# Performance work log

Measured on AMD Instinct MI355X. Metric: run time of the kernel, lower is better.

Reference implementation:

```python
import jax, jax.numpy as jnp
import numpy as np

N = 50000   # nodes
E = 600000  # edges (avg degree ~12)
R = 8       # num_relations = 2 * n_speakers**2, n_speakers=2
B = 32      # num_bases = args.batch_size
GD, H1, H2 = 128, 128, 128


def setup_inputs() -> dict:
    key = jax.random.key(0)
    ks = jax.random.split(key, 16)
    w = lambda k, shape: jax.random.normal(k, shape, jnp.float32) * 0.05
    return {
        "node_features": jax.random.normal(ks[0], (N, GD), jnp.float32),
        "edge_index": jax.random.randint(ks[1], (2, E), 0, N),
        "edge_norm": jax.random.uniform(ks[2], (E,), jnp.float32),
        "edge_type": jax.random.randint(ks[3], (E,), 0, R),
        "basis": w(ks[4], (B, GD, H1)),
        "comp": w(ks[5], (R, B)),
        "root": w(ks[6], (GD, H1)),
        "bias1": jnp.zeros((H1,), jnp.float32),
        "w_key": w(ks[7], (H1, H2)),
        "b_key": jnp.zeros((H2,), jnp.float32),
        "w_query": w(ks[8], (H1, H2)),
        "b_query": jnp.zeros((H2,), jnp.float32),
        "w_value": w(ks[9], (H1, H2)),
        "b_value": jnp.zeros((H2,), jnp.float32),
        "w_skip": w(ks[10], (H1, H2)),
        "b_skip": jnp.zeros((H2,), jnp.float32),
    }


def reference(node_features, edge_index, edge_norm, edge_type, basis, comp,
              root, bias1, w_key, b_key, w_query, b_query, w_value, b_value,
              w_skip, b_skip):
    n = node_features.shape[0]
    r = comp.shape[0]
    src, dst = edge_index[0], edge_index[1]

    # ---- RGCNConv (basis decomposition, per-relation mean aggregation) ----
    W = jnp.einsum('rb,bio->rio', comp, basis)            # [R, GD, H1]
    xW = jnp.einsum('ni,rio->rno', node_features, W)      # [R, N, H1]
    msg = xW[edge_type, src]                              # [E, H1]
    seg = edge_type * n + dst                             # combined (relation, dst) segment id
    agg = jax.ops.segment_sum(msg, seg, num_segments=r * n).reshape(r, n, -1)
    cnt = jax.ops.segment_sum(jnp.ones(msg.shape[0], jnp.float32), seg,
                              num_segments=r * n).reshape(r, n, 1)
    h = (agg / jnp.maximum(cnt, 1.0)).sum(0) + node_features @ root + bias1

    # ---- ResGatedGraphConv: sigmoid(k_i + q_j) * v_j, sum-aggregated + skip ----
    k = h @ w_key + b_key
    q = h @ w_query + b_query
    v = h @ w_value + b_value
    m = jax.nn.sigmoid(k[dst] + q[src]) * v[src]          # [E, H2]
    out = jax.ops.segment_sum(m, dst, num_segments=n) + h @ w_skip + b_skip
    return out
```

## Files before the change

### kernel.cpp

```cpp
#include <hip/hip_runtime.h>
#include <stdint.h>

#define GD 128
#define H1 128
#define H2 128
#define NBASES 32
#define NREL 8
#define KA 1152

typedef __attribute__((ext_vector_type(8))) short bf16x8;
typedef __attribute__((ext_vector_type(4))) float f32x4;

static inline size_t align256(size_t x){ return (x + 255) & ~(size_t)255; }

__device__ __forceinline__ float bf2f(uint32_t u16){
  union { uint32_t u; float f; } c; c.u = (u16 & 0xffffu) << 16; return c.f;
}
__device__ __forceinline__ unsigned short f2bf(float f){
  union { float f; uint32_t u; } c; c.f = f;
  uint32_t u = c.u;
  u += 0x7fffu + ((u >> 16) & 1u);
  return (unsigned short)(u >> 16);
}
__device__ __forceinline__ uint32_t pkbf(float a, float b){
  union { float f; uint32_t u; } ca, cb; ca.f = a; cb.f = b;
  return __builtin_amdgcn_perm(cb.u + 0x8000u, ca.u + 0x8000u, 0x07060302u);
}

__device__ __forceinline__ void async_copy16(void* lds_dst, const void* gsrc){
  __builtin_amdgcn_global_load_lds(
      (const __attribute__((address_space(1))) uint32_t*)gsrc,
      (__attribute__((address_space(3))) uint32_t*)lds_dst, 16, 0, 0);
}

__global__ void k_prep(const float* __restrict__ comp, const float* __restrict__ basis,
                       const float* __restrict__ root, unsigned short* __restrict__ Bht,
                       const float* __restrict__ wk, const float* __restrict__ wq,
                       const float* __restrict__ wv, const float* __restrict__ wsk,
                       const float* __restrict__ bk, const float* __restrict__ bq,
                       const float* __restrict__ bv, const float* __restrict__ bs,
                       unsigned short* __restrict__ B2t, float* __restrict__ Bb,
                       const float4* __restrict__ x, uint2* __restrict__ xout, int cnt4,
                       uint32_t* __restrict__ xpadz, int npadz,
                       const int* __restrict__ edst, const int* __restrict__ etyp,
                       int* __restrict__ cnt, int E, int n){
  const float LOG2E = 1.4426950408889634f;
  int b = blockIdx.x, t = threadIdx.x;
  if (b < 576){
    int idx = b*256 + t;
    int row = idx >> 7, i = idx & 127;
    int r = row >> 7, o = row & 127;
    float v;
    if (r < 8){
      float acc = 0.f;
      #pragma unroll
      for (int bb = 0; bb < NBASES; ++bb)
        acc += comp[r*NBASES + bb] * basis[((size_t)bb*GD + i)*H1 + o];
      v = acc;
    } else {
      v = root[(size_t)i*H1 + o];
    }
    Bht[(size_t)o*KA + r*128 + i] = f2bf(v);
  } else if (b < 576 + 256){
    int idx = (b - 576)*256 + t;
    int c = idx / H1, k = idx % H1;
    const float* w = (c < 128) ? wk : (c < 256) ? wq : (c < 384) ? wv : wsk;
    float val = w[(size_t)k*H2 + (c & 127)];
    if (c < 256) val *= LOG2E;
    B2t[idx] = f2bf(val);
    if (idx < 512){
      const float* bia = (idx < 128) ? bk : (idx < 256) ? bq : (idx < 384) ? bv : bs;
      float bval = bia[idx & 127];
      if (idx < 256) bval *= LOG2E;
      Bb[idx] = bval;
    }
  } else {
    int cb = b - (576 + 256);
    int ncastb = (cnt4 + 255) >> 8;
    if (cb < ncastb){
      int i = cb*256 + t;
      if (i < cnt4){
        float4 v = x[i];
        uint2 o; o.x = pkbf(v.x, v.y); o.y = pkbf(v.z, v.w);
        xout[i] = o;
      }
    } else if (cb < ncastb + 12){
      int i = (cb - ncastb)*256 + t;
      if (i < npadz) xpadz[i] = 0u;
    } else {
      int e = (cb - ncastb - 12)*256 + t;
      if (e < E) atomicAdd(&cnt[etyp[e]*n + edst[e]], 1);
    }
  }
}

__global__ void k_scanA(const int* __restrict__ deg, int* __restrict__ off,
                        int* __restrict__ btot, int len){
  __shared__ int wsum[16];
  int t = threadIdx.x, lane = t & 63, w = t >> 6;
  int i0 = blockIdx.x*8192 + t*8;
  int v[8];
  if (i0 + 7 < len){
    int4 va = *(const int4*)(deg + i0);
    int4 vb = *(const int4*)(deg + i0 + 4);
    v[0]=va.x; v[1]=va.y; v[2]=va.z; v[3]=va.w;
    v[4]=vb.x; v[5]=vb.y; v[6]=vb.z; v[7]=vb.w;
  } else {
    #pragma unroll
    for (int u = 0; u < 8; ++u) v[u] = (i0+u < len) ? deg[i0+u] : 0;
  }
  int s[8]; s[0] = v[0];
  #pragma unroll
  for (int u = 1; u < 8; ++u) s[u] = s[u-1] + v[u];
  int x = s[7];
  #pragma unroll
  for (int d = 1; d < 64; d <<= 1){
    int u = __shfl_up(x, d, 64);
    if (lane >= d) x += u;
  }
  if (lane == 63) wsum[w] = x;
  __syncthreads();
  if (t < 16){
    int y = wsum[t];
    #pragma unroll
    for (int d = 1; d < 16; d <<= 1){
      int u = __shfl_up(y, d, 16);
      if (t >= d) y += u;
    }
    wsum[t] = y;
  }
  __syncthreads();
  int woff = (w > 0) ? wsum[w-1] : 0;
  int excl = woff + x - s[7];
  #pragma unroll
  for (int u = 0; u < 8; ++u)
    if (i0+u < len) off[i0+u] = excl + s[u] - v[u];
  if (t == 0) btot[blockIdx.x] = wsum[15];
}

__global__ void k_scanB(const int* __restrict__ btot, int* __restrict__ off,
                        int* __restrict__ cursor, int len, int sentinel){
  int t = threadIdx.x, bid = blockIdx.x;
  int add = 0;
  for (int j = 0; j < bid; ++j) add += btot[j];
  int i0 = bid*8192 + t*8;
  #pragma unroll
  for (int u = 0; u < 8; ++u){
    int i = i0 + u;
    if (i < len){ int val = off[i] + add; off[i] = val; cursor[i] = val; }
  }
  if (bid == 0 && t == 0) off[len] = sentinel;
}

__global__ void k_scatter_rd(const int* __restrict__ src, const int* __restrict__ dst,
                             const int* __restrict__ typ, int* __restrict__ cursor,
                             int* __restrict__ pk, int E, int n){
  int e = blockIdx.x*blockDim.x + threadIdx.x;
  if (e >= E) return;
  int pos = atomicAdd(&cursor[typ[e]*n + dst[e]], 1);
  pk[pos] = src[e];
}

__global__ void k_agg(const int* __restrict__ off_rd, const int* __restrict__ pk_rd,
                      const uint32_t* __restrict__ x32, unsigned short* __restrict__ A2,
                      int n, int npad){
  int wid = blockIdx.x*(blockDim.x >> 6) + (threadIdx.x >> 6);
  int lane = threadIdx.x & 63;
  if (wid >= npad) return;
  uint32_t* arow = (uint32_t*)(A2 + (size_t)wid*1024);
  if (wid >= n){
    #pragma unroll
    for (int u = 0; u < 8; ++u) arow[u*64 + lane] = 0u;
    return;
  }
  int r8 = lane & 7;
  int o_r = off_rd[(size_t)r8*n + wid];
  int e_r = off_rd[(size_t)r8*n + wid + 1];
  int c_r = e_r - o_r;
  float ic_r = (c_r > 0) ? __builtin_amdgcn_rcpf((float)c_r) : 0.f;
  int c0_ = __builtin_amdgcn_readlane(c_r, 0), c1_ = __builtin_amdgcn_readlane(c_r, 1);
  int c2_ = __builtin_amdgcn_readlane(c_r, 2), c3_ = __builtin_amdgcn_readlane(c_r, 3);
  int c4_ = __builtin_amdgcn_readlane(c_r, 4), c5_ = __builtin_amdgcn_readlane(c_r, 5);
  int c6_ = __builtin_amdgcn_readlane(c_r, 6), c7_ = __builtin_amdgcn_readlane(c_r, 7);
  int o0_ = __builtin_amdgcn_readlane(o_r, 0), o1_ = __builtin_amdgcn_readlane(o_r, 1);
  int o2_ = __builtin_amdgcn_readlane(o_r, 2), o3_ = __builtin_amdgcn_readlane(o_r, 3);
  int o4_ = __builtin_amdgcn_readlane(o_r, 4), o5_ = __builtin_amdgcn_readlane(o_r, 5);
  int o6_ = __builtin_amdgcn_readlane(o_r, 6), o7_ = __builtin_amdgcn_readlane(o_r, 7);
  int p1 = c0_, p2 = p1 + c1_, p3 = p2 + c2_, p4 = p3 + c3_;
  int p5 = p4 + c4_, p6 = p5 + c5_, p7 = p6 + c6_, dg = p7 + c7_;

  int cr = 0;
  float a0 = 0.f, a1 = 0.f;

#define FLUSH(RK)                                                               \
  {                                                                             \
    float ic = __int_as_float(__builtin_amdgcn_readlane(__float_as_int(ic_r), cr)); \
    arow[cr*64 + lane] = pkbf(a0*ic, a1*ic);                                    \
    for (int q = cr + 1; q < (RK); ++q) arow[q*64 + lane] = 0u;                 \
    cr = (RK); a0 = 0.f; a1 = 0.f;                                              \
  }

  for (int jb = 0; jb < dg; jb += 64){
    int i = jb + lane;
    int adj = o0_, rel = 0;
    adj = (i >= p1) ? (o1_ - p1) : adj;  rel += (i >= p1);
    adj = (i >= p2) ? (o2_ - p2) : adj;  rel += (i >= p2);
    adj = (i >= p3) ? (o3_ - p3) : adj;  rel += (i >= p3);
    adj = (i >= p4) ? (o4_ - p4) : adj;  rel += (i >= p4);
    adj = (i >= p5) ? (o5_ - p5) : adj;  rel += (i >= p5);
    adj = (i >= p6) ? (o6_ - p6) : adj;  rel += (i >= p6);
    adj = (i >= p7) ? (o7_ - p7) : adj;  rel += (i >= p7);
    int m = dg - jb; if (m > 64) m = 64;
    int pj = (lane < m) ? pk_rd[adj + i] : 0;
    int jj = 0;
    for (; jj + 8 <= m; jj += 8){
      uint32_t g[8];
      #pragma unroll
      for (int k = 0; k < 8; ++k){
        int sN = __builtin_amdgcn_readlane(pj, jj + k);
        g[k] = x32[(size_t)(uint32_t)sN*64 + lane];
      }
      #pragma unroll
      for (int k = 0; k < 8; ++k){
        int rk = __builtin_amdgcn_readlane(rel, jj + k);
        if (rk != cr) FLUSH(rk);
        a0 += bf2f(g[k]); a1 += bf2f(g[k] >> 16);
      }
    }
    for (; jj < m; jj += 4){
      int lim = m - 1;
      uint32_t g[4];
      #pragma unroll
      for (int k = 0; k < 4; ++k){
        int tt = jj + k; if (tt > lim) tt = lim;
        int sN = __builtin_amdgcn_readlane(pj, tt);
        g[k] = x32[(size_t)(uint32_t)sN*64 + lane];
      }
      #pragma unroll
      for (int k = 0; k < 4; ++k){
        int tt = jj + k;
        if (tt < m){
          int rk = __builtin_amdgcn_readlane(rel, tt);
          if (rk != cr) FLUSH(rk);
          a0 += bf2f(g[k]); a1 += bf2f(g[k] >> 16);
        }
      }
    }
  }
  FLUSH(8)
#undef FLUSH
}

__launch_bounds__(256)
__global__ void k_hgemm(const unsigned short* __restrict__ A, const unsigned short* __restrict__ xb,
                        const unsigned short* __restrict__ Bt,
                        const float* __restrict__ bias1, unsigned short* __restrict__ h){
  __shared__ char lds[16896];
  int t = threadIdx.x, lane = t & 63, wave = t >> 6;
  int row0 = blockIdx.x * 128;
  int mrow = lane & 15, quad = lane >> 4;
  int wrow = (wave & 1) * 64, wcol = (wave >> 1) * 64;
  int s = (mrow >> 1) & 3;
  int colsw = (((t & 3) ^ ((t >> 3) & 3)) << 3);

  const unsigned short* Asrc = A  + (size_t)(row0 + (t >> 2))*1024 + colsw;
  const unsigned short* Xsrc = xb + (size_t)(row0 + (t >> 2))*GD   + colsw;
  const unsigned short* Bsrc = Bt + (size_t)(t >> 2)*KA + colsw;
  char* ldsw = lds + wave*1024;

  int aoff = (wrow + mrow)*64 + ((quad ^ s) << 4);
  int boff = 8192 + (wcol + mrow)*64 + ((quad ^ s) << 4);

  f32x4 acc[4][4];
  #pragma unroll
  for (int i = 0; i < 4; ++i)
    #pragma unroll
    for (int j = 0; j < 4; ++j) acc[i][j] = (f32x4){0.f,0.f,0.f,0.f};

  for (int kt = 0; kt < KA; kt += 32){
    const unsigned short* a0p = (kt < 1024) ? (Asrc + kt)
                                            : (Xsrc + (kt - 1024));
    const unsigned short* a1p = (kt < 1024) ? (Asrc + (size_t)64*1024 + kt)
                                            : (Xsrc + (size_t)64*GD + (kt - 1024));
    __syncthreads();
    async_copy16(ldsw,         a0p);
    async_copy16(ldsw + 4096,  a1p);
    async_copy16(ldsw + 8192,  Bsrc + kt);
    async_copy16(ldsw + 12288, Bsrc + (size_t)64*KA + kt);
    __syncthreads();
    bf16x8 af[4], bf[4];
    #pragma unroll
    for (int i = 0; i < 4; ++i) af[i] = *(const bf16x8*)(lds + aoff + i*1024);
    #pragma unroll
    for (int j = 0; j < 4; ++j) bf[j] = *(const bf16x8*)(lds + boff + j*1024);
    #pragma unroll
    for (int i = 0; i < 4; ++i)
      #pragma unroll
      for (int j = 0; j < 4; ++j)
        acc[i][j] = __builtin_amdgcn_mfma_f32_16x16x32_bf16(af[i], bf[j], acc[i][j], 0, 0, 0);
  }
  float bc[4];
  #pragma unroll
  for (int j = 0; j < 4; ++j) bc[j] = bias1[wcol + j*16 + mrow];
  #pragma unroll
  for (int p = 0; p < 2; ++p){
    __syncthreads();
    if ((wave & 1) == p){
      #pragma unroll
      for (int j = 0; j < 4; ++j){
        int col = wcol + j*16 + mrow;
        #pragma unroll
        for (int i = 0; i < 4; ++i)
          #pragma unroll
          for (int rg = 0; rg < 4; ++rg){
            int rl = i*16 + quad*4 + rg;
            *(unsigned short*)(lds + rl*264 + col*2) = f2bf(acc[i][j][rg] + bc[j]);
          }
      }
    }
    __syncthreads();
    uint32_t vv[16];
    #pragma unroll
    for (int u = 0; u < 8; ++u)
      *(uint2*)&vv[u*2] = *(const uint2*)(lds + lane*264 + wave*64 + u*8);
    unsigned short* gp = h + (size_t)(row0 + p*64 + lane)*H1 + wave*32;
    #pragma unroll
    for (int u = 0; u < 4; ++u)
      *(uint4*)(gp + u*8) = *(const uint4*)&vv[u*4];
  }
}

__launch_bounds__(256)
__global__ void k_gemm2(const unsigned short* __restrict__ A, const unsigned short* __restrict__ Bt,
                        const float* __restrict__ Bb, unsigned short* __restrict__ kqv,
                        unsigned short* __restrict__ skipb){
  __shared__ char lds[16896];
  int t = threadIdx.x, lane = t & 63, wave = t >> 6;
  int row0 = blockIdx.x * 128;
  int c0 = blockIdx.y * 128;
  int mrow = lane & 15, quad = lane >> 4;
  int wrow = (wave & 1) * 64, wcol = (wave >> 1) * 64;
  int s = (mrow >> 1) & 3;

  const unsigned short* Asrc = A + (size_t)(row0 + (t >> 2))*H1 + (((t & 3) ^ ((t >> 3) & 3)) << 3);
  const unsigned short* Bsrc = Bt + (size_t)(c0 + (t >> 2))*H1 + (((t & 3) ^ ((t >> 3) & 3)) << 3);
  char* ldsw = lds + wave*1024;

  int aoff = (wrow + mrow)*64 + ((quad ^ s) << 4);
  int boff = 8192 + (wcol + mrow)*64 + ((quad ^ s) << 4);

  f32x4 acc[4][4];
  #pragma unroll
  for (int i = 0; i < 4; ++i)
    #pragma unroll
    for (int j = 0; j < 4; ++j) acc[i][j] = (f32x4){0.f,0.f,0.f,0.f};

  #pragma unroll
  for (int kt = 0; kt < H1; kt += 32){
    __syncthreads();
    async_copy16(ldsw,         Asrc + kt);
    async_copy16(ldsw + 4096,  Asrc + (size_t)64*H1 + kt);
    async_copy16(ldsw + 8192,  Bsrc + kt);
    async_copy16(ldsw + 12288, Bsrc + (size_t)64*H1 + kt);
    __syncthreads();
    bf16x8 af[4], bf[4];
    #pragma unroll
    for (int i = 0; i < 4; ++i) af[i] = *(const bf16x8*)(lds + aoff + i*1024);
    #pragma unroll
    for (int j = 0; j < 4; ++j) bf[j] = *(const bf16x8*)(lds + boff + j*1024);
    #pragma unroll
    for (int i = 0; i < 4; ++i)
      #pragma unroll
      for (int j = 0; j < 4; ++j)
        acc[i][j] = __builtin_amdgcn_mfma_f32_16x16x32_bf16(af[i], bf[j], acc[i][j], 0, 0, 0);
  }
  float bc[4];
  #pragma unroll
  for (int j = 0; j < 4; ++j) bc[j] = Bb[c0 + wcol + j*16 + mrow];
  unsigned short* dstb; size_t ldu;
  if (c0 < 384){ dstb = kqv + c0; ldu = 384; } else { dstb = skipb; ldu = 128; }
  #pragma unroll
  for (int p = 0; p < 2; ++p){
    __syncthreads();
    if ((wave & 1) == p){
      #pragma unroll
      for (int j = 0; j < 4; ++j){
        int col = wcol + j*16 + mrow;
        #pragma unroll
        for (int i = 0; i < 4; ++i)
          #pragma unroll
          for (int rg = 0; rg < 4; ++rg){
            int rl = i*16 + quad*4 + rg;
            *(unsigned short*)(lds + rl*264 + col*2) = f2bf(acc[i][j][rg] + bc[j]);
          }
      }
    }
    __syncthreads();
    uint32_t vv[16];
    #pragma unroll
    for (int u = 0; u < 8; ++u)
      *(uint2*)&vv[u*2] = *(const uint2*)(lds + lane*264 + wave*64 + u*8);
    unsigned short* gp = dstb + (size_t)(row0 + p*64 + lane)*ldu + wave*32;
    #pragma unroll
    for (int u = 0; u < 4; ++u)
      *(uint4*)(gp + u*8) = *(const uint4*)&vv[u*4];
  }
}

__global__ void k_edge2(const int* __restrict__ off_rd, const int* __restrict__ pk_rd,
                        const unsigned short* __restrict__ kqv,
                        const unsigned short* __restrict__ skipb,
                        float* __restrict__ out, int n){
  int wid = blockIdx.x*(blockDim.x >> 6) + (threadIdx.x >> 6);
  int lane = threadIdx.x & 63;
  if (wid >= n) return;
  const uint32_t* kv32 = (const uint32_t*)kqv;
  int r = lane & 7;
  int o_r = off_rd[(size_t)r*n + wid];
  int e_r = off_rd[(size_t)r*n + wid + 1];
  int c_r = e_r - o_r;
  int c0_ = __builtin_amdgcn_readlane(c_r, 0), c1_ = __builtin_amdgcn_readlane(c_r, 1);
  int c2_ = __builtin_amdgcn_readlane(c_r, 2), c3_ = __builtin_amdgcn_readlane(c_r, 3);
  int c4_ = __builtin_amdgcn_readlane(c_r, 4), c5_ = __builtin_amdgcn_readlane(c_r, 5);
  int c6_ = __builtin_amdgcn_readlane(c_r, 6), c7_ = __builtin_amdgcn_readlane(c_r, 7);
  int o0_ = __builtin_amdgcn_readlane(o_r, 0), o1_ = __builtin_amdgcn_readlane(o_r, 1);
  int o2_ = __builtin_amdgcn_readlane(o_r, 2), o3_ = __builtin_amdgcn_readlane(o_r, 3);
  int o4_ = __builtin_amdgcn_readlane(o_r, 4), o5_ = __builtin_amdgcn_readlane(o_r, 5);
  int o6_ = __builtin_amdgcn_readlane(o_r, 6), o7_ = __builtin_amdgcn_readlane(o_r, 7);
  int p1 = c0_, p2 = p1 + c1_, p3 = p2 + c2_, p4 = p3 + c3_;
  int p5 = p4 + c4_, p6 = p5 + c5_, p7 = p6 + c6_, dg = p7 + c7_;

  uint32_t ku = kv32[(size_t)wid*192 + lane];
  float k0 = bf2f(ku), k1 = bf2f(ku >> 16);
  float a0 = 0.f, a1 = 0.f;
  for (int jb = 0; jb < dg; jb += 64){
    int i = jb + lane;
    int adj = o0_;
    adj = (i >= p1) ? (o1_ - p1) : adj;
    adj = (i >= p2) ? (o2_ - p2) : adj;
    adj = (i >= p3) ? (o3_ - p3) : adj;
    adj = (i >= p4) ? (o4_ - p4) : adj;
    adj = (i >= p5) ? (o5_ - p5) : adj;
    adj = (i >= p6) ? (o6_ - p6) : adj;
    adj = (i >= p7) ? (o7_ - p7) : adj;
    int m = dg - jb; if (m > 64) m = 64;
    int pj = (lane < m) ? pk_rd[adj + i] : 0;
    int jj = 0;
    for (; jj + 8 <= m; jj += 8){
      uint32_t qg[8], vg[8];
      #pragma unroll
      for (int k = 0; k < 8; ++k){
        int s = __builtin_amdgcn_readlane(pj, jj + k);
        const uint32_t* rowp = kv32 + (size_t)s*192 + lane;
        qg[k] = rowp[64];
        vg[k] = rowp[128];
      }
      #pragma unroll
      for (int k = 0; k < 8; ++k){
        float qq0 = bf2f(qg[k]), qq1 = bf2f(qg[k] >> 16);
        float vv0 = bf2f(vg[k]), vv1 = bf2f(vg[k] >> 16);
        float g0 = __builtin_amdgcn_rcpf(1.f + __builtin_amdgcn_exp2f(-(k0 + qq0)));
        float g1 = __builtin_amdgcn_rcpf(1.f + __builtin_amdgcn_exp2f(-(k1 + qq1)));
        a0 += g0*vv0; a1 += g1*vv1;
      }
    }
    for (; jj + 4 <= m; jj += 4){
      uint32_t qg[4], vg[4];
      #pragma unroll
      for (int k = 0; k < 4; ++k){
        int s = __builtin_amdgcn_readlane(pj, jj + k);
        const uint32_t* rowp = kv32 + (size_t)s*192 + lane;
        qg[k] = rowp[64];
        vg[k] = rowp[128];
      }
      #pragma unroll
      for (int k = 0; k < 4; ++k){
        float qq0 = bf2f(qg[k]), qq1 = bf2f(qg[k] >> 16);
        float vv0 = bf2f(vg[k]), vv1 = bf2f(vg[k] >> 16);
        float g0 = __builtin_amdgcn_rcpf(1.f + __builtin_amdgcn_exp2f(-(k0 + qq0)));
        float g1 = __builtin_amdgcn_rcpf(1.f + __builtin_amdgcn_exp2f(-(k1 + qq1)));
        a0 += g0*vv0; a1 += g1*vv1;
      }
    }
    for (; jj < m; ++jj){
      int s = __builtin_amdgcn_readlane(pj, jj);
      const uint32_t* rowp = kv32 + (size_t)s*192 + lane;
      uint32_t qg = rowp[64], vg = rowp[128];
      float qq0 = bf2f(qg), qq1 = bf2f(qg >> 16);
      float vv0 = bf2f(vg), vv1 = bf2f(vg >> 16);
      float g0 = __builtin_amdgcn_rcpf(1.f + __builtin_amdgcn_exp2f(-(k0 + qq0)));
      float g1 = __builtin_amdgcn_rcpf(1.f + __builtin_amdgcn_exp2f(-(k1 + qq1)));
      a0 += g0*vv0; a1 += g1*vv1;
    }
  }
  uint32_t sk = ((const uint32_t*)skipb)[(size_t)wid*64 + lane];
  float2 cur; cur.x = a0 + bf2f(sk); cur.y = a1 + bf2f(sk >> 16);
  ((float2*)(out + (size_t)wid*H2))[lane] = cur;
}

extern "C" void kernel_launch(void* const* d_in, const int* in_sizes, int n_in,
                              void* d_out, int out_size, void* d_ws, size_t ws_size,
                              hipStream_t stream){
  const float* x     = (const float*)d_in[0];
  const int*   eidx  = (const int*)  d_in[1];
  const int*   etype = (const int*)  d_in[3];
  const float* basis = (const float*)d_in[4];
  const float* comp  = (const float*)d_in[5];
  const float* root  = (const float*)d_in[6];
  const float* bias1 = (const float*)d_in[7];
  const float* wk    = (const float*)d_in[8];
  const float* bk    = (const float*)d_in[9];
  const float* wq    = (const float*)d_in[10];
  const float* bq    = (const float*)d_in[11];
  const float* wv    = (const float*)d_in[12];
  const float* bv    = (const float*)d_in[13];
  const float* wsk   = (const float*)d_in[14];
  const float* bs    = (const float*)d_in[15];
  const int n = in_sizes[0] / GD;
  const int E = in_sizes[3];
  const int npad = (n + 127) & ~127;
  const int* esrc = eidx;
  const int* edst = eidx + E;
  float* out = (float*)d_out;

  char* w = (char*)d_ws;
  size_t off = 0;
  unsigned short* xbf  = (unsigned short*)(w + off); off = align256(off + (size_t)npad*GD*2);
  unsigned short* A2   = (unsigned short*)(w + off); off = align256(off + (size_t)npad*1024*2);
  unsigned short* Bht  = (unsigned short*)(w + off); off = align256(off + (size_t)KA*H1*2);
  unsigned short* B2t  = (unsigned short*)(w + off); off = align256(off + (size_t)512*H1*2);
  float* Bb            = (float*)(w + off);          off = align256(off + 512*4);
  unsigned short* hbuf = (unsigned short*)(w + off); off = align256(off + (size_t)npad*H1*2);
  unsigned short* kqv  = (unsigned short*)(w + off); off = align256(off + (size_t)npad*384*2);
  unsigned short* skipb= (unsigned short*)(w + off); off = align256(off + (size_t)npad*H2*2);
  int* cnt_rd          = (int*)(w + off);            off = align256(off + (size_t)(8*n+4)*4);
  int* off_rd          = (int*)(w + off);            off = align256(off + (size_t)(8*n+1)*4);
  int* cur_rd          = (int*)(w + off);            off = align256(off + (size_t)8*n*4);
  int* btot_rd         = (int*)(w + off);            off = align256(off + 64*4);
  int* pk_rd           = (int*)(w + off);            off = align256(off + (size_t)E*4);

  const int nblk_rd = (8*n + 8191) / 8192;
  const int cnt4 = n*GD/4;
  const int ncastb = (cnt4 + 255)/256;
  const int histb  = (E + 255)/256;
  const int npadz  = (npad - n)*GD/2;

  hipMemsetAsync(cnt_rd, 0, (size_t)8*n*4, stream);

  k_prep<<<576 + 256 + ncastb + 12 + histb, 256, 0, stream>>>(
      comp, basis, root, Bht, wk, wq, wv, wsk, bk, bq, bv, bs, B2t, Bb,
      (const float4*)x, (uint2*)xbf, cnt4,
      (uint32_t*)(xbf + (size_t)n*GD), npadz,
      edst, etype, cnt_rd, E, n);
  k_scanA<<<nblk_rd, 1024, 0, stream>>>(cnt_rd, off_rd, btot_rd, 8*n);
  k_scanB<<<nblk_rd, 1024, 0, stream>>>(btot_rd, off_rd, cur_rd, 8*n, E);
  k_scatter_rd<<<(E + 255)/256, 256, 0, stream>>>(esrc, edst, etype, cur_rd, pk_rd, E, n);
  k_agg<<<(npad + 3)/4, 256, 0, stream>>>(off_rd, pk_rd, (const uint32_t*)xbf, A2, n, npad);
  k_hgemm<<<npad/128, 256, 0, stream>>>(A2, xbf, Bht, bias1, hbuf);
  k_gemm2<<<dim3(npad/128, 4), 256, 0, stream>>>(hbuf, B2t, Bb, kqv, skipb);
  k_edge2<<<(n + 3)/4, 256, 0, stream>>>(off_rd, pk_rd, kqv, skipb, out, n);
}
```

Measured before the change: 352.2 us.

## Fuse per-relation mean aggregation into the h GEMM via LDS tiles

Replaces the separate aggregation kernel, which wrote a large [npad,1024] bf16 buffer A2, with a fused kernel. Each block aggregates its 128 nodes one relation at a time into a swizzled LDS tile and immediately feeds it to the MFMA GEMM against that relation's weight slice, then handles the root term from x. This removes the A2 global write and re-read. In exchange the block count drops to npad/128, so there are far fewer waves to hide the gather latency, and LDS use grows to 48KB per block. The prep kernel is also restructured so the basis composition reuses the loaded basis values across relations, and the bf16 cast now does 4 elements per thread.

```diff
diff --git a/kernel.cpp b/kernel.cpp
--- a/kernel.cpp
+++ b/kernel.cpp
@@ -25,6 +25,9 @@
 __device__ __forceinline__ uint32_t pkbf(float a, float b){
   union { float f; uint32_t u; } ca, cb; ca.f = a; cb.f = b;
   return __builtin_amdgcn_perm(cb.u + 0x8000u, ca.u + 0x8000u, 0x07060302u);
+}
+__device__ __forceinline__ float rdlanef(float v, int l){
+  return __int_as_float(__builtin_amdgcn_readlane(__float_as_int(v), l));
 }
 
 __device__ __forceinline__ void async_copy16(void* lds_dst, const void* gsrc){
@@ -46,23 +49,25 @@
                        int* __restrict__ cnt, int E, int n){
   const float LOG2E = 1.4426950408889634f;
   int b = blockIdx.x, t = threadIdx.x;
-  if (b < 576){
-    int idx = b*256 + t;
-    int row = idx >> 7, i = idx & 127;
-    int r = row >> 7, o = row & 127;
-    float v;
-    if (r < 8){
+  if (b < 128){
+    int i = b;
+    int o = t & 127, rh = t >> 7;
+    float bv[NBASES];
+    #pragma unroll
+    for (int bb = 0; bb < NBASES; ++bb)
+      bv[bb] = basis[((size_t)bb*GD + i)*H1 + o];
+    #pragma unroll
+    for (int rr = 0; rr < 4; ++rr){
+      int r = rh*4 + rr;
       float acc = 0.f;
       #pragma unroll
       for (int bb = 0; bb < NBASES; ++bb)
-        acc += comp[r*NBASES + bb] * basis[((size_t)bb*GD + i)*H1 + o];
-      v = acc;
-    } else {
-      v = root[(size_t)i*H1 + o];
-    }
-    Bht[(size_t)o*KA + r*128 + i] = f2bf(v);
-  } else if (b < 576 + 256){
-    int idx = (b - 576)*256 + t;
+        acc += comp[r*NBASES + bb] * bv[bb];
+      Bht[(size_t)o*KA + r*128 + i] = f2bf(acc);
+    }
+    if (rh == 1) Bht[(size_t)o*KA + 1024 + i] = f2bf(root[(size_t)i*H1 + o]);
+  } else if (b < 128 + 256){
+    int idx = (b - 128)*256 + t;
     int c = idx / H1, k = idx % H1;
     const float* w = (c < 128) ? wk : (c < 256) ? wq : (c < 384) ? wv : wsk;
     float val = w[(size_t)k*H2 + (c & 127)];
@@ -75,14 +80,18 @@
       Bb[idx] = bval;
     }
   } else {
-    int cb = b - (576 + 256);
-    int ncastb = (cnt4 + 255) >> 8;
+    int cb = b - (128 + 256);
+    int ncastb = (cnt4 + 1023) >> 10;
     if (cb < ncastb){
-      int i = cb*256 + t;
-      if (i < cnt4){
-        float4 v = x[i];
-        uint2 o; o.x = pkbf(v.x, v.y); o.y = pkbf(v.z, v.w);
-        xout[i] = o;
+      int base = cb*1024 + t;
+      #pragma unroll
+      for (int u = 0; u < 4; ++u){
+        int i = base + u*256;
+        if (i < cnt4){
+          float4 v = x[i];
+          uint2 o; o.x = pkbf(v.x, v.y); o.y = pkbf(v.z, v.w);
+          xout[i] = o;
+        }
       }
     } else if (cb < ncastb + 12){
       int i = (cb - ncastb)*256 + t;
@@ -161,101 +170,12 @@
   pk[pos] = src[e];
 }
 
-__global__ void k_agg(const int* __restrict__ off_rd, const int* __restrict__ pk_rd,
-                      const uint32_t* __restrict__ x32, unsigned short* __restrict__ A2,
-                      int n, int npad){
-  int wid = blockIdx.x*(blockDim.x >> 6) + (threadIdx.x >> 6);
-  int lane = threadIdx.x & 63;
-  if (wid >= npad) return;
-  uint32_t* arow = (uint32_t*)(A2 + (size_t)wid*1024);
-  if (wid >= n){
-    #pragma unroll
-    for (int u = 0; u < 8; ++u) arow[u*64 + lane] = 0u;
-    return;
-  }
-  int r8 = lane & 7;
-  int o_r = off_rd[(size_t)r8*n + wid];
-  int e_r = off_rd[(size_t)r8*n + wid + 1];
-  int c_r = e_r - o_r;
-  float ic_r = (c_r > 0) ? __builtin_amdgcn_rcpf((float)c_r) : 0.f;
-  int c0_ = __builtin_amdgcn_readlane(c_r, 0), c1_ = __builtin_amdgcn_readlane(c_r, 1);
-  int c2_ = __builtin_amdgcn_readlane(c_r, 2), c3_ = __builtin_amdgcn_readlane(c_r, 3);
-  int c4_ = __builtin_amdgcn_readlane(c_r, 4), c5_ = __builtin_amdgcn_readlane(c_r, 5);
-  int c6_ = __builtin_amdgcn_readlane(c_r, 6), c7_ = __builtin_amdgcn_readlane(c_r, 7);
-  int o0_ = __builtin_amdgcn_readlane(o_r, 0), o1_ = __builtin_amdgcn_readlane(o_r, 1);
-  int o2_ = __builtin_amdgcn_readlane(o_r, 2), o3_ = __builtin_amdgcn_readlane(o_r, 3);
-  int o4_ = __builtin_amdgcn_readlane(o_r, 4), o5_ = __builtin_amdgcn_readlane(o_r, 5);
-  int o6_ = __builtin_amdgcn_readlane(o_r, 6), o7_ = __builtin_amdgcn_readlane(o_r, 7);
-  int p1 = c0_, p2 = p1 + c1_, p3 = p2 + c2_, p4 = p3 + c3_;
-  int p5 = p4 + c4_, p6 = p5 + c5_, p7 = p6 + c6_, dg = p7 + c7_;
-
-  int cr = 0;
-  float a0 = 0.f, a1 = 0.f;
-
-#define FLUSH(RK)                                                               \
-  {                                                                             \
-    float ic = __int_as_float(__builtin_amdgcn_readlane(__float_as_int(ic_r), cr)); \
-    arow[cr*64 + lane] = pkbf(a0*ic, a1*ic);                                    \
-    for (int q = cr + 1; q < (RK); ++q) arow[q*64 + lane] = 0u;                 \
-    cr = (RK); a0 = 0.f; a1 = 0.f;                                              \
-  }
-
-  for (int jb = 0; jb < dg; jb += 64){
-    int i = jb + lane;
-    int adj = o0_, rel = 0;
-    adj = (i >= p1) ? (o1_ - p1) : adj;  rel += (i >= p1);
-    adj = (i >= p2) ? (o2_ - p2) : adj;  rel += (i >= p2);
-    adj = (i >= p3) ? (o3_ - p3) : adj;  rel += (i >= p3);
-    adj = (i >= p4) ? (o4_ - p4) : adj;  rel += (i >= p4);
-    adj = (i >= p5) ? (o5_ - p5) : adj;  rel += (i >= p5);
-    adj = (i >= p6) ? (o6_ - p6) : adj;  rel += (i >= p6);
-    adj = (i >= p7) ? (o7_ - p7) : adj;  rel += (i >= p7);
-    int m = dg - jb; if (m > 64) m = 64;
-    int pj = (lane < m) ? pk_rd[adj + i] : 0;
-    int jj = 0;
-    for (; jj + 8 <= m; jj += 8){
-      uint32_t g[8];
-      #pragma unroll
-      for (int k = 0; k < 8; ++k){
-        int sN = __builtin_amdgcn_readlane(pj, jj + k);
-        g[k] = x32[(size_t)(uint32_t)sN*64 + lane];
-      }
-      #pragma unroll
-      for (int k = 0; k < 8; ++k){
-        int rk = __builtin_amdgcn_readlane(rel, jj + k);
-        if (rk != cr) FLUSH(rk);
-        a0 += bf2f(g[k]); a1 += bf2f(g[k] >> 16);
-      }
-    }
-    for (; jj < m; jj += 4){
-      int lim = m - 1;
-      uint32_t g[4];
-      #pragma unroll
-      for (int k = 0; k < 4; ++k){
-        int tt = jj + k; if (tt > lim) tt = lim;
-        int sN = __builtin_amdgcn_readlane(pj, tt);
-        g[k] = x32[(size_t)(uint32_t)sN*64 + lane];
-      }
-      #pragma unroll
-      for (int k = 0; k < 4; ++k){
-        int tt = jj + k;
-        if (tt < m){
-          int rk = __builtin_amdgcn_readlane(rel, tt);
-          if (rk != cr) FLUSH(rk);
-          a0 += bf2f(g[k]); a1 += bf2f(g[k] >> 16);
-        }
-      }
-    }
-  }
-  FLUSH(8)
-#undef FLUSH
-}
-
 __launch_bounds__(256)
-__global__ void k_hgemm(const unsigned short* __restrict__ A, const unsigned short* __restrict__ xb,
-                        const unsigned short* __restrict__ Bt,
-                        const float* __restrict__ bias1, unsigned short* __restrict__ h){
-  __shared__ char lds[16896];
+__global__ void k_fused(const int* __restrict__ off_rd, const int* __restrict__ pk_rd,
+                        const uint32_t* __restrict__ x32, const unsigned short* __restrict__ xb,
+                        const unsigned short* __restrict__ Bt, const float* __restrict__ bias1,
+                        unsigned short* __restrict__ h, int n){
+  __shared__ char lds[49152];
   int t = threadIdx.x, lane = t & 63, wave = t >> 6;
   int row0 = blockIdx.x * 128;
   int mrow = lane & 15, quad = lane >> 4;
@@ -263,13 +183,16 @@
   int s = (mrow >> 1) & 3;
   int colsw = (((t & 3) ^ ((t >> 3) & 3)) << 3);
 
-  const unsigned short* Asrc = A  + (size_t)(row0 + (t >> 2))*1024 + colsw;
-  const unsigned short* Xsrc = xb + (size_t)(row0 + (t >> 2))*GD   + colsw;
+  const unsigned short* Xsrc = xb + (size_t)(row0 + (t >> 2))*GD + colsw;
   const unsigned short* Bsrc = Bt + (size_t)(t >> 2)*KA + colsw;
-  char* ldsw = lds + wave*1024;
+  char* stage = lds + 32768;
+  char* ldsw = stage + wave*1024;
 
   int aoff = (wrow + mrow)*64 + ((quad ^ s) << 4);
   int boff = 8192 + (wcol + mrow)*64 + ((quad ^ s) << 4);
+  int axor = (mrow & 7) << 4;
+  int wbase = wave*32;
+  int d0 = row0 + wbase;
 
   f32x4 acc[4][4];
   #pragma unroll
@@ -277,27 +200,116 @@
     #pragma unroll
     for (int j = 0; j < 4; ++j) acc[i][j] = (f32x4){0.f,0.f,0.f,0.f};
 
-  for (int kt = 0; kt < KA; kt += 32){
-    const unsigned short* a0p = (kt < 1024) ? (Asrc + kt)
-                                            : (Xsrc + (kt - 1024));
-    const unsigned short* a1p = (kt < 1024) ? (Asrc + (size_t)64*1024 + kt)
-                                            : (Xsrc + (size_t)64*GD + (kt - 1024));
-    __syncthreads();
-    async_copy16(ldsw,         a0p);
-    async_copy16(ldsw + 4096,  a1p);
-    async_copy16(ldsw + 8192,  Bsrc + kt);
-    async_copy16(ldsw + 12288, Bsrc + (size_t)64*KA + kt);
-    __syncthreads();
-    bf16x8 af[4], bf[4];
-    #pragma unroll
-    for (int i = 0; i < 4; ++i) af[i] = *(const bf16x8*)(lds + aoff + i*1024);
-    #pragma unroll
-    for (int j = 0; j < 4; ++j) bf[j] = *(const bf16x8*)(lds + boff + j*1024);
-    #pragma unroll
-    for (int i = 0; i < 4; ++i)
-      #pragma unroll
-      for (int j = 0; j < 4; ++j)
-        acc[i][j] = __builtin_amdgcn_mfma_f32_16x16x32_bf16(af[i], bf[j], acc[i][j], 0, 0, 0);
+  for (int r = 0; r < 9; ++r){
+    if (r < 8){
+      __syncthreads();
+      int oidx = d0 + lane; if (oidx > n) oidx = n;
+      int ow = (lane < 33) ? off_rd[(size_t)r*n + oidx] : 0;
+      int ownx = __shfl_down(ow, 1, 64);
+      int cN = ownx - ow;
+      float icN = (cN > 0) ? __builtin_amdgcn_rcpf((float)cN) : 0.f;
+      int ebase = __builtin_amdgcn_readlane(ow, 0);
+      int segN  = __builtin_amdgcn_readlane(ow, 32) - ebase;
+      int pb[31];
+      #pragma unroll
+      for (int j = 0; j < 31; ++j)
+        pb[j] = __builtin_amdgcn_readlane(ow, j + 1) - ebase;
+
+      int cn = 0; float a0 = 0.f, a1 = 0.f;
+#define TFLUSH(RK)                                                               \
+      {                                                                          \
+        float ic = rdlanef(icN, cn);                                             \
+        *(uint32_t*)(lds + (wbase + cn)*256 + ((lane*4) ^ ((cn & 7) << 4)))      \
+            = pkbf(a0*ic, a1*ic);                                                \
+        for (int q2 = cn + 1; q2 < (RK); ++q2)                                   \
+          *(uint32_t*)(lds + (wbase + q2)*256 + ((lane*4) ^ ((q2 & 7) << 4)))    \
+              = 0u;                                                              \
+        cn = (RK); a0 = 0.f; a1 = 0.f;                                           \
+      }
+      for (int jb = 0; jb < segN; jb += 64){
+        int i = jb + lane;
+        int node = 0;
+        #pragma unroll
+        for (int j = 0; j < 31; ++j) node += (i >= pb[j]);
+        int m = segN - jb; if (m > 64) m = 64;
+        int pj = (lane < m) ? pk_rd[ebase + i] : 0;
+        int jj = 0;
+        for (; jj + 8 <= m; jj += 8){
+          uint32_t g[8];
+          #pragma unroll
+          for (int k = 0; k < 8; ++k){
+            int sN = __builtin_amdgcn_readlane(pj, jj + k);
+            g[k] = x32[(size_t)(uint32_t)sN*64 + lane];
+          }
+          #pragma unroll
+          for (int k = 0; k < 8; ++k){
+            int rk = __builtin_amdgcn_readlane(node, jj + k);
+            if (rk != cn) TFLUSH(rk);
+            a0 += bf2f(g[k]); a1 += bf2f(g[k] >> 16);
+          }
+        }
+        for (; jj < m; jj += 4){
+          int lim = m - 1;
+          uint32_t g[4];
+          #pragma unroll
+          for (int k = 0; k < 4; ++k){
+            int tt = jj + k; if (tt > lim) tt = lim;
+            int sN = __builtin_amdgcn_readlane(pj, tt);
+            g[k] = x32[(size_t)(uint32_t)sN*64 + lane];
+          }
+          #pragma unroll
+          for (int k = 0; k < 4; ++k){
+            int tt = jj + k;
+            if (tt < m){
+              int rk = __builtin_amdgcn_readlane(node, tt);
+              if (rk != cn) TFLUSH(rk);
+              a0 += bf2f(g[k]); a1 += bf2f(g[k] >> 16);
+            }
+          }
+        }
+      }
+      TFLUSH(32)
+#undef TFLUSH
+      __syncthreads();
+      for (int c4 = 0; c4 < 4; ++c4){
+        int kts = c4*32;
+        if (c4) __syncthreads();
+        async_copy16(ldsw + 8192,  Bsrc + r*128 + kts);
+        async_copy16(ldsw + 12288, Bsrc + (size_t)64*KA + r*128 + kts);
+        __syncthreads();
+        bf16x8 af[4], bf[4];
+        #pragma unroll
+        for (int i = 0; i < 4; ++i)
+          af[i] = *(const bf16x8*)(lds + (wrow + i*16 + mrow)*256 + (((kts + quad*8)*2) ^ axor));
+        #pragma unroll
+        for (int j = 0; j < 4; ++j) bf[j] = *(const bf16x8*)(stage + boff + j*1024);
+        #pragma unroll
+        for (int i = 0; i < 4; ++i)
+          #pragma unroll
+          for (int j = 0; j < 4; ++j)
+            acc[i][j] = __builtin_amdgcn_mfma_f32_16x16x32_bf16(af[i], bf[j], acc[i][j], 0, 0, 0);
+      }
+    } else {
+      for (int c4 = 0; c4 < 4; ++c4){
+        int kts = c4*32;
+        __syncthreads();
+        async_copy16(ldsw,         Xsrc + kts);
+        async_copy16(ldsw + 4096,  Xsrc + (size_t)64*GD + kts);
+        async_copy16(ldsw + 8192,  Bsrc + 1024 + kts);
+        async_copy16(ldsw + 12288, Bsrc + (size_t)64*KA + 1024 + kts);
+        __syncthreads();
+        bf16x8 af[4], bf[4];
+        #pragma unroll
+        for (int i = 0; i < 4; ++i) af[i] = *(const bf16x8*)(stage + aoff + i*1024);
+        #pragma unroll
+        for (int j = 0; j < 4; ++j) bf[j] = *(const bf16x8*)(stage + boff + j*1024);
+        #pragma unroll
+        for (int i = 0; i < 4; ++i)
+          #pragma unroll
+          for (int j = 0; j < 4; ++j)
+            acc[i][j] = __builtin_amdgcn_mfma_f32_16x16x32_bf16(af[i], bf[j], acc[i][j], 0, 0, 0);
+      }
+    }
   }
   float bc[4];
   #pragma unroll
@@ -526,7 +538,6 @@
   char* w = (char*)d_ws;
   size_t off = 0;
   unsigned short* xbf  = (unsigned short*)(w + off); off = align256(off + (size_t)npad*GD*2);
-  unsigned short* A2   = (unsigned short*)(w + off); off = align256(off + (size_t)npad*1024*2);
   unsigned short* Bht  = (unsigned short*)(w + off); off = align256(off + (size_t)KA*H1*2);
   unsigned short* B2t  = (unsigned short*)(w + off); off = align256(off + (size_t)512*H1*2);
   float* Bb            = (float*)(w + off);          off = align256(off + 512*4);
@@ -541,13 +552,13 @@
 
   const int nblk_rd = (8*n + 8191) / 8192;
   const int cnt4 = n*GD/4;
-  const int ncastb = (cnt4 + 255)/256;
+  const int ncastb = (cnt4 + 1023)/1024;
   const int histb  = (E + 255)/256;
   const int npadz  = (npad - n)*GD/2;
 
   hipMemsetAsync(cnt_rd, 0, (size_t)8*n*4, stream);
 
-  k_prep<<<576 + 256 + ncastb + 12 + histb, 256, 0, stream>>>(
+  k_prep<<<128 + 256 + ncastb + 12 + histb, 256, 0, stream>>>(
       comp, basis, root, Bht, wk, wq, wv, wsk, bk, bq, bv, bs, B2t, Bb,
       (const float4*)x, (uint2*)xbf, cnt4,
       (uint32_t*)(xbf + (size_t)n*GD), npadz,
@@ -555,8 +566,8 @@
   k_scanA<<<nblk_rd, 1024, 0, stream>>>(cnt_rd, off_rd, btot_rd, 8*n);
   k_scanB<<<nblk_rd, 1024, 0, stream>>>(btot_rd, off_rd, cur_rd, 8*n, E);
   k_scatter_rd<<<(E + 255)/256, 256, 0, stream>>>(esrc, edst, etype, cur_rd, pk_rd, E, n);
-  k_agg<<<(npad + 3)/4, 256, 0, stream>>>(off_rd, pk_rd, (const uint32_t*)xbf, A2, n, npad);
-  k_hgemm<<<npad/128, 256, 0, stream>>>(A2, xbf, Bht, bias1, hbuf);
+  k_fused<<<npad/128, 256, 0, stream>>>(off_rd, pk_rd, (const uint32_t*)xbf, xbf,
+                                        Bht, bias1, hbuf, n);
   k_gemm2<<<dim3(npad/128, 4), 256, 0, stream>>>(hbuf, B2t, Bb, kqv, skipb);
   k_edge2<<<(n + 3)/4, 256, 0, stream>>>(off_rd, pk_rd, kqv, skipb, out, n);
 }
```

Result: faster. 340.3 us (-3.4%).
